# Kernel tuning notes

Hardware: AMD Instinct MI355X
Metric: run time of the kernel (lower is better)

The kernel has to match this reference:

```python
import jax, jax.numpy as jnp
import numpy as np

B, NVARS, H, D_MODEL = 16, 32, 128, 128
N_HEADS, MERGE = 8, 2
HEAD_DIM = D_MODEL // N_HEADS
D_FF = 256
ALPHA = 0.3
EPS = 1e-5  # BatchNorm1d default eps


def make_ema(T, alpha):
    # row i: E[i,0]=(1-a)^i, E[i,j]=a*(1-a)^(i-j) for 1<=j<=i, 0 above diagonal
    i = np.arange(T)
    diff = i[:, None] - i[None, :]
    E = np.where(diff >= 0, alpha * (1.0 - alpha) ** np.maximum(diff, 0), 0.0)
    E[:, 0] = (1.0 - alpha) ** i
    return jnp.asarray(E, dtype=jnp.float32)


def batchnorm(x, gamma, beta):
    # x: [BN, L, C]; torch does Transpose(1,2)->BatchNorm1d(C)->Transpose(1,2),
    # i.e. normalize each channel over (batch, length) with biased variance (train mode).
    mean = x.mean(axis=(0, 1), keepdims=True)
    var = x.var(axis=(0, 1), keepdims=True)
    return (x - mean) * jax.lax.rsqrt(var + EPS) * gamma + beta


def merge_heads(x):
    # x: [B, N, heads, T, d]. Torch: reshape(B*N, heads*T, d) then
    # rearrange '(hl1 hl2 hl3) d -> hl2 (hl3 hl1) d' with hl1=heads//MERGE, hl2=T, hl3=MERGE,
    # then reshape(B*N, T, heads*d).
    b, n, h, t, d = x.shape
    hl1 = h // MERGE
    y = x.reshape(b * n, hl1, t, MERGE, d)
    y = y.transpose(0, 2, 3, 1, 4).reshape(b * n, t, h * d)
    return y


def setup_inputs() -> dict:
    key = jax.random.key(0)
    ks = jax.random.split(key, 8)
    s = lambda fan_in: 1.0 / np.sqrt(fan_in)
    return {
        "src": jax.random.normal(ks[0], (B, NVARS, H, D_MODEL), jnp.float32),
        "qkv_w": jax.random.normal(ks[1], (D_MODEL, 3 * D_MODEL), jnp.float32) * s(D_MODEL),
        "qkv_b": jnp.zeros((3 * D_MODEL,), jnp.float32),
        "ff1_w1": jax.random.normal(ks[2], (D_MODEL, D_FF), jnp.float32) * s(D_MODEL),
        "ff1_b1": jnp.zeros((D_FF,), jnp.float32),
        "ff1_w2": jax.random.normal(ks[3], (D_FF, D_MODEL), jnp.float32) * s(D_FF),
        "ff1_b2": jnp.zeros((D_MODEL,), jnp.float32),
        "ff2_w1": jax.random.normal(ks[4], (D_MODEL, D_FF), jnp.float32) * s(D_MODEL),
        "ff2_b1": jnp.zeros((D_FF,), jnp.float32),
        "ff2_w2": jax.random.normal(ks[5], (D_FF, D_MODEL), jnp.float32) * s(D_FF),
        "ff2_b2": jnp.zeros((D_MODEL,), jnp.float32),
        "g1": jnp.ones((D_MODEL,), jnp.float32), "b1": jnp.zeros((D_MODEL,), jnp.float32),
        "g2": jnp.ones((D_MODEL,), jnp.float32), "b2": jnp.zeros((D_MODEL,), jnp.float32),
        "g3": jnp.ones((D_MODEL,), jnp.float32), "b3": jnp.zeros((D_MODEL,), jnp.float32),
        "ema_mat": make_ema(H, ALPHA),
    }


def reference(src, qkv_w, qkv_b, ff1_w1, ff1_b1, ff1_w2, ff1_b2,
              ff2_w1, ff2_b1, ff2_w2, ff2_b2, g1, b1, g2, b2, g3, b3, ema_mat):
    Bc, Nc, T, C = src.shape
    qkv = (src @ qkv_w + qkv_b).reshape(Bc, Nc, T, 3, N_HEADS, HEAD_DIM)
    qkv = jnp.transpose(qkv, (3, 0, 1, 4, 2, 5))  # [3, B, N, heads, T, d]
    q, k, v = qkv[0], qkv[1], qkv[2]

    E = ema_mat[:T, :T]
    ema = lambda x: jnp.einsum('bnhad,ga->bnhgd', x, E)

    # NB: original divides by head_dim**(-0.5), i.e. multiplies by sqrt(head_dim)
    s_tok = jnp.einsum('bnhed,bnhfd->bnhef', ema(q), ema(k)) * (HEAD_DIM ** 0.5)
    a_tok = jax.nn.softmax(s_tok, axis=-1)            # dropout p=0 (eval)
    o_tok = jnp.einsum('bnhef,bnhfd->bnhed', a_tok, v)  # [B,N,h,T,d]

    # hidden-dim attention: scores are [d,d], contracted over tokens; scale by sqrt(T)
    s_hid = jnp.einsum('bnhae,bnhaf->bnhef', q, k) * (T ** 0.5)
    a_hid = jax.nn.softmax(s_hid, axis=-1)
    o_hid = jnp.einsum('bnhef,bnhaf->bnhae', a_hid, v)  # [B,N,h,T,d]

    out1 = batchnorm(merge_heads(o_tok), g1, b1).reshape(Bc, Nc, T, C)
    out2 = batchnorm(merge_heads(o_hid), g2, b2).reshape(Bc, Nc, T, C)

    ff = lambda x, w1, bb1, w2, bb2: jax.nn.gelu(x @ w1 + bb1, approximate=False) @ w2 + bb2
    src2 = ff(out1, ff1_w1, ff1_b1, ff1_w2, ff1_b2) + ff(out2, ff2_w1, ff2_b1, ff2_w2, ff2_b2)

    out = src + src2
    out = batchnorm(out.reshape(Bc * Nc, T, C), g3, b3).reshape(Bc, Nc, T, C)
    return out
```

## Files before the change

kernel.cpp:

```cpp
#include <hip/hip_runtime.h>
#include <math.h>

#define BN_ 512
#define T_  128
#define C_  128
#define H_  8
#define D_  16
#define F_  256
#define M_  65536

typedef __bf16 bf16x8 __attribute__((ext_vector_type(8)));
typedef float f32x4 __attribute__((ext_vector_type(4)));
union U8 { uint2 d[2]; bf16x8 v; unsigned short u[8]; };

__device__ inline unsigned short f2bf(float x) {
  union { float f; unsigned int u; } a; a.f = x;
  unsigned int r = a.u + 0x7fffu + ((a.u >> 16) & 1u);
  return (unsigned short)(r >> 16);
}
__device__ inline float bf2f(unsigned short h) {
  return __uint_as_float((unsigned int)h << 16);
}
__device__ inline float gelu_f(float x) {
  float z  = x * 0.70710678118654752f;
  float az = fabsf(z);
  float t  = 1.0f / (1.0f + 0.3275911f * az);
  float poly = ((((1.061405429f*t - 1.453152027f)*t + 1.421413741f)*t
                 - 0.284496736f)*t + 0.254829592f)*t;
  float e  = __expf(-z*z);
  float er = 1.0f - poly*e;
  er = (z < 0.0f) ? -er : er;
  return 0.5f * x * (1.0f + er);
}

__global__ __launch_bounds__(256, 4) void k_qkv(
    const float* __restrict__ src, const unsigned short* __restrict__ wqh,
    const unsigned short* __restrict__ wql, const float* __restrict__ bias,
    float* __restrict__ qb, float* __restrict__ kb, float* __restrict__ vb) {
  __shared__ __align__(16) unsigned short Ah[8*512], Al[8*512];
  const int tid = threadIdx.x;
  const int lane = tid & 63, w = tid >> 6;
  const int cl = lane & 15, g = lane >> 4;
  const size_t rb = (size_t)blockIdx.x * 32;

  #pragma unroll
  for (int it=0; it<4; ++it) {
    int idx = it*256 + tid;
    int r = idx >> 5, c4 = (idx & 31)*4;
    float4 v = *(const float4*)&src[(rb + r)*128 + c4];
    float vv[4] = {v.x, v.y, v.z, v.w};
    int s = c4 >> 5, kl = c4 & 31;
    int g2 = (kl >> 2) & 3, j0 = (kl >> 4) << 2;
    int fi = ((r>>4)*4 + s)*512 + (g2*16 + (r & 15))*8 + j0;
    unsigned short h4[4], l4[4];
    #pragma unroll
    for (int e=0;e<4;++e) {
      h4[e] = f2bf(vv[e]);
      l4[e] = f2bf(vv[e] - bf2f(h4[e]));
    }
    *(uint2*)&Ah[fi] = make_uint2((unsigned)h4[0] | ((unsigned)h4[1]<<16),
                                  (unsigned)h4[2] | ((unsigned)h4[3]<<16));
    *(uint2*)&Al[fi] = make_uint2((unsigned)l4[0] | ((unsigned)l4[1]<<16),
                                  (unsigned)l4[2] | ((unsigned)l4[3]<<16));
  }
  __syncthreads();

  f32x4 acc[2][6];
  #pragma unroll
  for (int m=0;m<2;++m)
    #pragma unroll
    for (int n=0;n<6;++n) acc[m][n] = 0;

  #pragma unroll
  for (int s=0; s<4; ++s) {
    bf16x8 ah[2], al[2];
    #pragma unroll
    for (int m=0;m<2;++m) {
      ah[m] = *(const bf16x8*)&Ah[(m*4+s)*512 + lane*8];
      al[m] = *(const bf16x8*)&Al[(m*4+s)*512 + lane*8];
    }
    #pragma unroll
    for (int nt=0; nt<6; ++nt) {
      int n = w*96 + nt*16 + cl;
      size_t fi = (size_t)((s*384 + n)*4 + g)*8;
      bf16x8 bh = *(const bf16x8*)(wqh + fi);
      bf16x8 bl = *(const bf16x8*)(wql + fi);
      #pragma unroll
      for (int m=0;m<2;++m) {
        acc[m][nt] = __builtin_amdgcn_mfma_f32_16x16x32_bf16(ah[m], bh, acc[m][nt], 0,0,0);
        acc[m][nt] = __builtin_amdgcn_mfma_f32_16x16x32_bf16(ah[m], bl, acc[m][nt], 0,0,0);
        acc[m][nt] = __builtin_amdgcn_mfma_f32_16x16x32_bf16(al[m], bh, acc[m][nt], 0,0,0);
      }
    }
  }

  #pragma unroll
  for (int nt=0; nt<6; ++nt) {
    int n = w*96 + nt*16 + cl;
    int which = n >> 7, loc = n & 127;
    int h = loc >> 4, d = loc & 15;
    float* outb = (which==0) ? qb : ((which==1) ? kb : vb);
    float bv = bias[n];
    #pragma unroll
    for (int m=0;m<2;++m) {
      #pragma unroll
      for (int r=0;r<4;++r) {
        size_t row = rb + m*16 + g*4 + r;
        int bn = (int)(row >> 7), t = (int)(row & 127);
        outb[(((size_t)(bn*8 + h))*128 + t)*16 + d] = acc[m][nt][r] + bv;
      }
    }
  }
}

__global__ __launch_bounds__(256, 4) void k_attn(
    const float* __restrict__ qb, const float* __restrict__ kb,
    const float* __restrict__ vb, const unsigned short* __restrict__ ef,
    unsigned short* __restrict__ o1b, unsigned short* __restrict__ o2b,
    float* __restrict__ p12) {
  __shared__ __align__(16) unsigned short QFh[2048], QFl[2048];
  __shared__ __align__(16) unsigned short KFh[2048], KFl[2048];
  __shared__ __align__(16) unsigned short VF[2048];
  __shared__ __align__(16) unsigned short Vn[128*20];
  __shared__ __align__(16) unsigned short eqL[128*20], ekL[128*20];
  __shared__ __align__(16) float s2L[16*17];
  __shared__ float part[128];
  const int tid = threadIdx.x;
  const int lane = tid & 63, w = tid >> 6;
  const int cl = lane & 15, g = lane >> 4;
  const int bn = blockIdx.x >> 3, h = blockIdx.x & 7;
  const int h1 = h >> 1, hb = h & 1;
  const size_t base = (size_t)(bn*8 + h) * 2048;

  if (tid < 128) part[tid] = 0.f;

  {
    const int t = tid >> 1, d0 = (tid & 1) * 8;
    const int s = t >> 5, kk = t & 31;
    const int g2 = (kk >> 2) & 3;
    const int j = ((kk >> 4) << 2) | (kk & 3);
    const float* qp = &qb[base + t*16 + d0];
    const float* kp = &kb[base + t*16 + d0];
    const float* vp = &vb[base + t*16 + d0];
    float4 qa = *(const float4*)qp, qc = *(const float4*)(qp+4);
    float4 ka = *(const float4*)kp, kc = *(const float4*)(kp+4);
    float4 va = *(const float4*)vp, vc = *(const float4*)(vp+4);
    float qv[8] = {qa.x,qa.y,qa.z,qa.w,qc.x,qc.y,qc.z,qc.w};
    float kv[8] = {ka.x,ka.y,ka.z,ka.w,kc.x,kc.y,kc.z,kc.w};
    float vv[8] = {va.x,va.y,va.z,va.w,vc.x,vc.y,vc.z,vc.w};
    unsigned short vh[8];
    #pragma unroll
    for (int e2=0;e2<8;++e2) {
      int fi = s*512 + (g2*16 + d0 + e2)*8 + j;
      unsigned short qh = f2bf(qv[e2]);
      QFh[fi] = qh; QFl[fi] = f2bf(qv[e2] - bf2f(qh));
      unsigned short kh = f2bf(kv[e2]);
      KFh[fi] = kh; KFl[fi] = f2bf(kv[e2] - bf2f(kh));
      vh[e2] = f2bf(vv[e2]);
      VF[fi] = vh[e2];
    }
    unsigned int p0 = (unsigned)vh[0] | ((unsigned)vh[1]<<16);
    unsigned int p1 = (unsigned)vh[2] | ((unsigned)vh[3]<<16);
    unsigned int p2 = (unsigned)vh[4] | ((unsigned)vh[5]<<16);
    unsigned int p3 = (unsigned)vh[6] | ((unsigned)vh[7]<<16);
    *(uint2*)&Vn[t*20 + d0]     = make_uint2(p0,p1);
    *(uint2*)&Vn[t*20 + d0 + 4] = make_uint2(p2,p3);
  }
  __syncthreads();

  {
    f32x4 aq[2], ak[2];
    #pragma unroll
    for (int m=0;m<2;++m){ aq[m]=0; ak[m]=0; }
    #pragma unroll
    for (int s=0;s<4;++s) {
      bf16x8 qf = *(const bf16x8*)&QFh[s*512 + lane*8];
      bf16x8 kf = *(const bf16x8*)&KFh[s*512 + lane*8];
      #pragma unroll
      for (int m=0;m<2;++m) {
        int mt = w*2 + m;
        bf16x8 eA = *(const bf16x8*)&ef[(size_t)((mt*4 + s)*64 + lane)*8];
        aq[m] = __builtin_amdgcn_mfma_f32_16x16x32_bf16(eA, qf, aq[m], 0,0,0);
        ak[m] = __builtin_amdgcn_mfma_f32_16x16x32_bf16(eA, kf, ak[m], 0,0,0);
      }
    }
    #pragma unroll
    for (int m=0;m<2;++m)
      #pragma unroll
      for (int r=0;r<4;++r) {
        int row = w*32 + m*16 + g*4 + r;
        eqL[row*20 + cl] = f2bf(aq[m][r]);
        ekL[row*20 + cl] = f2bf(ak[m][r]);
      }
  }
  if (w == 3) {
    f32x4 a2; a2 = 0;
    #pragma unroll
    for (int s=0;s<4;++s) {
      bf16x8 qh = *(const bf16x8*)&QFh[s*512 + lane*8];
      bf16x8 ql = *(const bf16x8*)&QFl[s*512 + lane*8];
      bf16x8 kh = *(const bf16x8*)&KFh[s*512 + lane*8];
      bf16x8 kl = *(const bf16x8*)&KFl[s*512 + lane*8];
      a2 = __builtin_amdgcn_mfma_f32_16x16x32_bf16(qh, kh, a2, 0,0,0);
      a2 = __builtin_amdgcn_mfma_f32_16x16x32_bf16(qh, kl, a2, 0,0,0);
      a2 = __builtin_amdgcn_mfma_f32_16x16x32_bf16(ql, kh, a2, 0,0,0);
    }
    #pragma unroll
    for (int r=0;r<4;++r) {
      float sv = a2[r] * 11.313708498984761f;
      float mx = sv;
      mx = fmaxf(mx, __shfl_xor(mx, 1));
      mx = fmaxf(mx, __shfl_xor(mx, 2));
      mx = fmaxf(mx, __shfl_xor(mx, 4));
      mx = fmaxf(mx, __shfl_xor(mx, 8));
      float p = __expf(sv - mx);
      float sum = p;
      sum += __shfl_xor(sum, 1);
      sum += __shfl_xor(sum, 2);
      sum += __shfl_xor(sum, 4);
      sum += __shfl_xor(sum, 8);
      s2L[(g*4 + r)*17 + cl] = p / sum;
    }
  }
  __syncthreads();

  {
    f32x4 accS[8][2];
    #pragma unroll
    for (int kt=0;kt<8;++kt)
      #pragma unroll
      for (int qt=0;qt<2;++qt) accS[kt][qt] = 0;
    U8 eb[2];
    #pragma unroll
    for (int qt=0;qt<2;++qt) {
      eb[qt].d[0] = *(const uint2*)&eqL[(w*32 + qt*16 + cl)*20 + 4*g];
      eb[qt].d[1] = make_uint2(0,0);
    }
    #pragma unroll
    for (int kt=0;kt<8;++kt) {
      U8 ea;
      ea.d[0] = *(const uint2*)&ekL[(kt*16 + cl)*20 + 4*g];
      ea.d[1] = make_uint2(0,0);
      #pragma unroll
      for (int qt=0;qt<2;++qt)
        accS[kt][qt] = __builtin_amdgcn_mfma_f32_16x16x32_bf16(ea.v, eb[qt].v, accS[kt][qt], 0,0,0);
    }
    bf16x8 vfr[4];
    #pragma unroll
    for (int s=0;s<4;++s) vfr[s] = *(const bf16x8*)&VF[s*512 + lane*8];
    #pragma unroll
    for (int qt=0;qt<2;++qt) {
      float mx = -1e30f;
      #pragma unroll
      for (int kt=0;kt<8;++kt)
        #pragma unroll
        for (int r=0;r<4;++r) {
          accS[kt][qt][r] *= 4.0f;
          mx = fmaxf(mx, accS[kt][qt][r]);
        }
      mx = fmaxf(mx, __shfl_xor(mx, 16));
      mx = fmaxf(mx, __shfl_xor(mx, 32));
      float sum = 0.f;
      #pragma unroll
      for (int kt=0;kt<8;++kt)
        #pragma unroll
        for (int r=0;r<4;++r) {
          float p = __expf(accS[kt][qt][r] - mx);
          accS[kt][qt][r] = p; sum += p;
        }
      sum += __shfl_xor(sum, 16);
      sum += __shfl_xor(sum, 32);
      float inv = 1.0f / sum;
      f32x4 o; o = 0;
      #pragma unroll
      for (int s=0;s<4;++s) {
        U8 pa;
        #pragma unroll
        for (int j=0;j<8;++j)
          pa.u[j] = f2bf(accS[2*s + (j>>2)][qt][j&3] * inv);
        o = __builtin_amdgcn_mfma_f32_16x16x32_bf16(pa.v, vfr[s], o, 0,0,0);
      }
      #pragma unroll
      for (int r=0;r<4;++r) {
        int e = w*32 + qt*16 + g*4 + r;
        int t2 = hb*64 + (e>>1), cb = (e&1)*64 + h1*16 + cl;
        o1b[((size_t)(bn*128 + t2))*128 + cb] = f2bf(o[r]);
      }
      float s0 = o[0]+o[2], q0 = o[0]*o[0]+o[2]*o[2];
      float s1 = o[1]+o[3], q1 = o[1]*o[1]+o[3]*o[3];
      s0 += __shfl_xor(s0,16); s0 += __shfl_xor(s0,32);
      q0 += __shfl_xor(q0,16); q0 += __shfl_xor(q0,32);
      s1 += __shfl_xor(s1,16); s1 += __shfl_xor(s1,32);
      q1 += __shfl_xor(q1,16); q1 += __shfl_xor(q1,32);
      if (g == 0) {
        atomicAdd(&part[cl],      s0);
        atomicAdd(&part[16+cl],   q0);
        atomicAdd(&part[32+cl],   s1);
        atomicAdd(&part[48+cl],   q1);
      }
    }
  }

  {
    U8 bb;
    #pragma unroll
    for (int j=0;j<4;++j) bb.u[j] = f2bf(s2L[cl*17 + 4*g + j]);
    bb.d[1] = make_uint2(0,0);
    #pragma unroll
    for (int m=0;m<2;++m) {
      int tt = w*2 + m;
      U8 va;
      va.d[0] = *(const uint2*)&Vn[(tt*16 + cl)*20 + 4*g];
      va.d[1] = make_uint2(0,0);
      f32x4 o; o = 0;
      o = __builtin_amdgcn_mfma_f32_16x16x32_bf16(va.v, bb.v, o, 0,0,0);
      #pragma unroll
      for (int r=0;r<4;++r) {
        int t = tt*16 + g*4 + r;
        int t2 = hb*64 + (t>>1), cb = (t&1)*64 + h1*16 + cl;
        o2b[((size_t)(bn*128 + t2))*128 + cb] = f2bf(o[r]);
      }
      float s0 = o[0]+o[2], q0 = o[0]*o[0]+o[2]*o[2];
      float s1 = o[1]+o[3], q1 = o[1]*o[1]+o[3]*o[3];
      s0 += __shfl_xor(s0,16); s0 += __shfl_xor(s0,32);
      q0 += __shfl_xor(q0,16); q0 += __shfl_xor(q0,32);
      s1 += __shfl_xor(s1,16); s1 += __shfl_xor(s1,32);
      q1 += __shfl_xor(q1,16); q1 += __shfl_xor(q1,32);
      if (g == 0) {
        atomicAdd(&part[64+cl],    s0);
        atomicAdd(&part[64+16+cl], q0);
        atomicAdd(&part[64+32+cl], s1);
        atomicAdd(&part[64+48+cl], q1);
      }
    }
  }
  __syncthreads();
  if (tid < 128) p12[(size_t)blockIdx.x*128 + tid] = part[tid];
}

__global__ __launch_bounds__(256) void k_red12(
    const float* __restrict__ p12, float* __restrict__ q12) {
  __shared__ float red[256];
  const int tid = threadIdx.x;
  const int slot = tid & 127, half = tid >> 7;
  const int h = blockIdx.x & 7, chunk = blockIdx.x >> 3;
  float s = 0.f;
  for (int t = half; t < 32; t += 2)
    s += p12[(size_t)((chunk*32 + t)*8 + h)*128 + slot];
  red[tid] = s;
  __syncthreads();
  if (tid < 128)
    q12[(size_t)blockIdx.x*128 + tid] = red[tid] + red[tid + 128];
}

__global__ __launch_bounds__(256) void k_fin12(
    const float* __restrict__ q12,
    const float* __restrict__ g1, const float* __restrict__ b1,
    const float* __restrict__ g2, const float* __restrict__ b2,
    float* __restrict__ stats) {
  const int tid = threadIdx.x;
  const int br = tid >> 7, c = tid & 127;
  const int grp = c >> 6, h1 = (c & 63) >> 4, cl = c & 15;
  const int slot = br*64 + grp*32 + cl;
  float s = 0.f, q = 0.f;
  #pragma unroll 4
  for (int chunk = 0; chunk < 16; ++chunk) {
    const float* p0 = &q12[(size_t)(chunk*8 + h1*2)*128];
    s += p0[slot]      + p0[128 + slot];
    q += p0[slot + 16] + p0[128 + slot + 16];
  }
  const float inv = 1.0f/65536.0f;
  float m = s*inv, v = q*inv - m*m;
  float r = rsqrtf(v + 1e-5f);
  float gv = br ? g2[c] : g1[c];
  float bv = br ? b2[c] : b1[c];
  float sc = r * gv;
  stats[br*256 + c]       = sc;
  stats[br*256 + 128 + c] = bv - m*sc;
}

__global__ __launch_bounds__(256) void k_prep(
    const float* __restrict__ w11, const float* __restrict__ w12,
    const float* __restrict__ w21, const float* __restrict__ w22,
    const float* __restrict__ ema, const float* __restrict__ qkvw,
    unsigned short* __restrict__ wf, unsigned short* __restrict__ ef,
    unsigned short* __restrict__ wqh, unsigned short* __restrict__ wql) {
  if (blockIdx.x >= 72) {
    int tid3 = (blockIdx.x - 72)*256 + threadIdx.x;
    int s = tid3 / 1536;
    int rem = tid3 - s*1536;
    int n = rem >> 2, g = rem & 3;
    size_t fi = (size_t)((s*384 + n)*4 + g)*8;
    #pragma unroll
    for (int j=0;j<8;++j) {
      int k = 32*s + 16*(j>>2) + 4*g + (j&3);
      float v = qkvw[(size_t)k*384 + n];
      unsigned short h = f2bf(v);
      wqh[fi+j] = h;
      wql[fi+j] = f2bf(v - bf2f(h));
    }
    return;
  }
  if (blockIdx.x >= 64) {
    int tid2 = (blockIdx.x - 64)*256 + threadIdx.x;
    int mt = tid2 >> 8, s = (tid2 >> 6) & 3, lane = tid2 & 63;
    int cl = lane & 15, g = lane >> 4;
    unsigned short* dst = ef + (size_t)tid2*8;
    #pragma unroll
    for (int j=0;j<8;++j) {
      int k = 32*s + 16*(j>>2) + 4*g + (j&3);
      dst[j] = f2bf(ema[(size_t)(mt*16 + cl)*128 + k]);
    }
    return;
  }
  int tid = blockIdx.x*256 + threadIdx.x;
  int m = tid >> 12;
  int idx = tid & 4095;
  const float* w; int N;
  if (m==0)      { w = w11; N = 256; }
  else if (m==1) { w = w12; N = 128; }
  else if (m==2) { w = w21; N = 256; }
  else           { w = w22; N = 128; }
  int g  = idx & 3;
  int sn = idx >> 2;
  int n  = (N==256) ? (sn & 255) : (sn & 127);
  int s  = (N==256) ? (sn >> 8)  : (sn >> 7);
  unsigned short* dst = wf + m*32768 + idx*8;
  #pragma unroll
  for (int j=0; j<8; ++j) {
    int k = s*32 + g*4 + (j&3) + 16*(j>>2);
    dst[j] = f2bf(w[(size_t)k*N + n]);
  }
}

__global__ void k_ff(
    const unsigned short* __restrict__ o1b, const unsigned short* __restrict__ o2b,
    const float* __restrict__ src,
    const float* __restrict__ bb11, const float* __restrict__ bb12,
    const float* __restrict__ bb21, const float* __restrict__ bb22,
    const unsigned short* __restrict__ wf,
    const float* __restrict__ stats, float* __restrict__ outp,
    float* __restrict__ p3) {
  __shared__ __align__(16) unsigned short Xbf[64*128];
  __shared__ __align__(16) unsigned short Hbf[64*128];
  const int tid = threadIdx.x;
  const int lane = tid & 63, w = tid >> 6;
  const int cl = lane & 15, g = lane >> 4;
  const size_t rb = (size_t)blockIdx.x * 64;

  f32x4 acc2[4];
  #pragma unroll
  for (int m=0;m<4;++m) acc2[m] = 0;

  for (int br=0; br<2; ++br) {
    const unsigned short* xin = br ? o2b : o1b;
    const float* sc_ = stats + br*256;
    const float* sh_ = sc_ + 128;
    const unsigned short* w1f = wf + br*65536;
    const unsigned short* w2f = w1f + 32768;
    const float* b1g = br ? bb21 : bb11;

    __syncthreads();
    #pragma unroll
    for (int it=0; it<4; ++it) {
      int idx = it*512 + tid;
      int row = idx >> 5, c4 = (idx & 31)*4;
      uint2 u = *(const uint2*)&xin[(rb+row)*128 + c4];
      float x0 = bf2f((unsigned short)(u.x & 0xffff));
      float x1 = bf2f((unsigned short)(u.x >> 16));
      float x2 = bf2f((unsigned short)(u.y & 0xffff));
      float x3 = bf2f((unsigned short)(u.y >> 16));
      unsigned int lo = f2bf(fmaf(x0, sc_[c4+0], sh_[c4+0]))
                      | ((unsigned int)f2bf(fmaf(x1, sc_[c4+1], sh_[c4+1])) << 16);
      unsigned int hi = f2bf(fmaf(x2, sc_[c4+2], sh_[c4+2]))
                      | ((unsigned int)f2bf(fmaf(x3, sc_[c4+3], sh_[c4+3])) << 16);
      unsigned int byteo = (unsigned)((row*256 + c4*2) ^ ((row&7)<<4));
      *(uint2*)((char*)Xbf + byteo) = make_uint2(lo, hi);
    }
    __syncthreads();

    #pragma unroll
    for (int hc=0; hc<2; ++hc) {
      f32x4 acc1[4];
      #pragma unroll
      for (int m=0;m<4;++m) acc1[m] = 0;

      bf16x8 bfs[4];
      #pragma unroll
      for (int s=0; s<4; ++s) {
        int n = hc*128 + w*16 + cl;
        bfs[s] = *(const bf16x8*)(w1f + (size_t)((s*256 + n)*4 + g)*8);
      }
      #pragma unroll
      for (int s=0; s<4; ++s) {
        #pragma unroll
        for (int m=0; m<4; ++m) {
          int row = m*16 + cl;
          U8 u;
          u.d[0] = *(uint2*)((char*)Xbf + (unsigned)((row*256 + (s*32 + g*4)*2)    ^ ((row&7)<<4)));
          u.d[1] = *(uint2*)((char*)Xbf + (unsigned)((row*256 + (s*32 +16+ g*4)*2) ^ ((row&7)<<4)));
          acc1[m] = __builtin_amdgcn_mfma_f32_16x16x32_bf16(u.v, bfs[s], acc1[m], 0, 0, 0);
        }
      }

      {
        int col = w*16 + cl;
        float bias = b1g[hc*128 + col];
        #pragma unroll
        for (int m=0; m<4; ++m) {
          #pragma unroll
          for (int r=0; r<4; ++r) {
            float y = gelu_f(acc1[m][r] + bias);
            int row = m*16 + g*4 + r;
            unsigned int byteo = (unsigned)((row*256 + col*2) ^ ((row&7)<<4));
            *(unsigned short*)((char*)Hbf + byteo) = f2bf(y);
          }
        }
      }
      __syncthreads();

      bf16x8 bf2[4];
      #pragma unroll
      for (int s2l=0; s2l<4; ++s2l) {
        int s2 = hc*4 + s2l;
        int n = w*16 + cl;
        bf2[s2l] = *(const bf16x8*)(w2f + (size_t)((s2*128 + n)*4 + g)*8);
      }
      #pragma unroll
      for (int s2l=0; s2l<4; ++s2l) {
        #pragma unroll
        for (int m=0; m<4; ++m) {
          int row = m*16 + cl;
          U8 u;
          u.d[0] = *(uint2*)((char*)Hbf + (unsigned)((row*256 + (s2l*32 + g*4)*2)    ^ ((row&7)<<4)));
          u.d[1] = *(uint2*)((char*)Hbf + (unsigned)((row*256 + (s2l*32 +16+ g*4)*2) ^ ((row&7)<<4)));
          acc2[m] = __builtin_amdgcn_mfma_f32_16x16x32_bf16(u.v, bf2[s2l], acc2[m], 0, 0, 0);
        }
      }
      __syncthreads();
    }
  }

  {
    int col = w*16 + cl;
    float bias = bb12[col] + bb22[col];
    float cs = 0.f, cq = 0.f;
    #pragma unroll
    for (int m=0; m<4; ++m) {
      #pragma unroll
      for (int r=0; r<4; ++r) {
        size_t row = rb + m*16 + g*4 + r;
        float o = src[row*128 + col] + acc2[m][r] + bias;
        outp[row*128 + col] = o;
        cs += o; cq = fmaf(o, o, cq);
      }
    }
    cs += __shfl_down(cs, 32); cs += __shfl_down(cs, 16);
    cq += __shfl_down(cq, 32); cq += __shfl_down(cq, 16);
    if (g == 0) {
      p3[(size_t)blockIdx.x*256 + col]       = cs;
      p3[(size_t)blockIdx.x*256 + 128 + col] = cq;
    }
  }
}

__global__ __launch_bounds__(256) void k_red3(
    const float* __restrict__ p3, float* __restrict__ q3) {
  const int tid = threadIdx.x;
  float s = 0.f;
  const int b0 = blockIdx.x*32;
  for (int b = b0; b < b0 + 32; ++b)
    s += p3[(size_t)b*256 + tid];
  q3[(size_t)blockIdx.x*256 + tid] = s;
}

__global__ __launch_bounds__(256) void k_fin3(
    const float* __restrict__ q3, const float* __restrict__ g3,
    const float* __restrict__ b3, float* __restrict__ stats) {
  __shared__ float acc[256];
  const int tid = threadIdx.x;
  float s = 0.f;
  #pragma unroll 4
  for (int i = 0; i < 32; ++i) s += q3[i*256 + tid];
  acc[tid] = s;
  __syncthreads();
  if (tid < 128) {
    const float inv = 1.0f/65536.0f;
    float m = acc[tid]*inv, v = acc[128+tid]*inv - m*m;
    float r = rsqrtf(v + 1e-5f);
    float scv = r*g3[tid];
    stats[512 + tid] = scv;
    stats[640 + tid] = b3[tid] - m*scv;
  }
}

__global__ __launch_bounds__(256) void k_bn3(
    float* __restrict__ outp, const float* __restrict__ stats) {
  const int i0 = blockIdx.x*256 + threadIdx.x;
  #pragma unroll
  for (int it=0; it<4; ++it) {
    size_t fi = ((size_t)i0 + (size_t)it*524288) * 4;
    int c = (int)(fi & 127);
    float4 v = *(float4*)&outp[fi];
    v.x = fmaf(v.x, stats[512+c+0], stats[640+c+0]);
    v.y = fmaf(v.y, stats[512+c+1], stats[640+c+1]);
    v.z = fmaf(v.z, stats[512+c+2], stats[640+c+2]);
    v.w = fmaf(v.w, stats[512+c+3], stats[640+c+3]);
    *(float4*)&outp[fi] = v;
  }
}

extern "C" void kernel_launch(void* const* d_in, const int* in_sizes, int n_in,
                              void* d_out, int out_size, void* d_ws, size_t ws_size,
                              hipStream_t stream) {
  const float* src   = (const float*)d_in[0];
  const float* qkv_w = (const float*)d_in[1];
  const float* qkv_b = (const float*)d_in[2];
  const float* ff1w1 = (const float*)d_in[3];
  const float* ff1b1 = (const float*)d_in[4];
  const float* ff1w2 = (const float*)d_in[5];
  const float* ff1b2 = (const float*)d_in[6];
  const float* ff2w1 = (const float*)d_in[7];
  const float* ff2b1 = (const float*)d_in[8];
  const float* ff2w2 = (const float*)d_in[9];
  const float* ff2b2 = (const float*)d_in[10];
  const float* g1 = (const float*)d_in[11];
  const float* b1 = (const float*)d_in[12];
  const float* g2 = (const float*)d_in[13];
  const float* b2 = (const float*)d_in[14];
  const float* g3 = (const float*)d_in[15];
  const float* b3 = (const float*)d_in[16];
  const float* ema = (const float*)d_in[17];

  float* ws = (float*)d_ws;
  float* qb  = ws;
  float* kb  = qb + 8388608;
  float* vb  = kb + 8388608;
  unsigned short* o1b = (unsigned short*)(vb + 8388608);
  unsigned short* o2b = o1b + 8388608;
  float* p12 = (float*)(o2b + 8388608);
  float* p3  = p12 + 524288;
  float* stats = p3 + 262144;
  unsigned short* wfrag = (unsigned short*)(stats + 1024);
  unsigned short* efrag = wfrag + 131072;
  unsigned short* wqh   = efrag + 16384;
  unsigned short* wql   = wqh + 49152;
  float* q12 = (float*)(wql + 49152);
  float* q3  = q12 + 16384;
  float* outp = (float*)d_out;

  k_prep<<<dim3(96), dim3(256), 0, stream>>>(ff1w1, ff1w2, ff2w1, ff2w2, ema,
                                             qkv_w, wfrag, efrag, wqh, wql);
  k_qkv<<<dim3(2048), dim3(256), 0, stream>>>(src, wqh, wql, qkv_b, qb, kb, vb);
  k_attn<<<dim3(4096), dim3(256), 0, stream>>>(qb, kb, vb, efrag, o1b, o2b, p12);
  k_red12<<<dim3(128), dim3(256), 0, stream>>>(p12, q12);
  k_fin12<<<dim3(1), dim3(256), 0, stream>>>(q12, g1, b1, g2, b2, stats);
  k_ff<<<dim3(1024), dim3(512), 0, stream>>>(o1b, o2b, src,
      ff1b1, ff1b2, ff2b1, ff2b2, wfrag, stats, outp, p3);
  k_red3<<<dim3(32), dim3(256), 0, stream>>>(p3, q3);
  k_fin3<<<dim3(1), dim3(256), 0, stream>>>(q3, g3, b3, stats);
  k_bn3<<<dim3(2048), dim3(256), 0, stream>>>(outp, stats);
}
```

Before: 210.0 us.

## Fuse QKV projection into attention kernel, dropping fp32 q/k/v round trip

The QKV projection kernel is merged into the attention kernel. Each block now computes the Q, K and V columns for its own (bn, head) directly from src and writes them as bf16 fragments into shared memory, so the fp32 q/k/v buffers are never stored to or read back from global memory. Block indices are remapped so that the 8 heads of one bn run on nearby blocks, which should let src rows be reused from cache. In exchange, src is read once per head (eight times in total), each block does more work, and shared memory use grows through the pooled staging buffers, which may lower occupancy.

```diff
diff --git a/kernel.cpp b/kernel.cpp
--- a/kernel.cpp
+++ b/kernel.cpp
@@ -33,138 +33,97 @@
   return 0.5f * x * (1.0f + er);
 }
 
-__global__ __launch_bounds__(256, 4) void k_qkv(
-    const float* __restrict__ src, const unsigned short* __restrict__ wqh,
-    const unsigned short* __restrict__ wql, const float* __restrict__ bias,
-    float* __restrict__ qb, float* __restrict__ kb, float* __restrict__ vb) {
-  __shared__ __align__(16) unsigned short Ah[8*512], Al[8*512];
-  const int tid = threadIdx.x;
-  const int lane = tid & 63, w = tid >> 6;
-  const int cl = lane & 15, g = lane >> 4;
-  const size_t rb = (size_t)blockIdx.x * 32;
-
-  #pragma unroll
-  for (int it=0; it<4; ++it) {
-    int idx = it*256 + tid;
-    int r = idx >> 5, c4 = (idx & 31)*4;
-    float4 v = *(const float4*)&src[(rb + r)*128 + c4];
-    float vv[4] = {v.x, v.y, v.z, v.w};
-    int s = c4 >> 5, kl = c4 & 31;
-    int g2 = (kl >> 2) & 3, j0 = (kl >> 4) << 2;
-    int fi = ((r>>4)*4 + s)*512 + (g2*16 + (r & 15))*8 + j0;
-    unsigned short h4[4], l4[4];
-    #pragma unroll
-    for (int e=0;e<4;++e) {
-      h4[e] = f2bf(vv[e]);
-      l4[e] = f2bf(vv[e] - bf2f(h4[e]));
-    }
-    *(uint2*)&Ah[fi] = make_uint2((unsigned)h4[0] | ((unsigned)h4[1]<<16),
-                                  (unsigned)h4[2] | ((unsigned)h4[3]<<16));
-    *(uint2*)&Al[fi] = make_uint2((unsigned)l4[0] | ((unsigned)l4[1]<<16),
-                                  (unsigned)l4[2] | ((unsigned)l4[3]<<16));
-  }
-  __syncthreads();
-
-  f32x4 acc[2][6];
-  #pragma unroll
-  for (int m=0;m<2;++m)
-    #pragma unroll
-    for (int n=0;n<6;++n) acc[m][n] = 0;
-
-  #pragma unroll
-  for (int s=0; s<4; ++s) {
-    bf16x8 ah[2], al[2];
-    #pragma unroll
-    for (int m=0;m<2;++m) {
-      ah[m] = *(const bf16x8*)&Ah[(m*4+s)*512 + lane*8];
-      al[m] = *(const bf16x8*)&Al[(m*4+s)*512 + lane*8];
-    }
-    #pragma unroll
-    for (int nt=0; nt<6; ++nt) {
-      int n = w*96 + nt*16 + cl;
-      size_t fi = (size_t)((s*384 + n)*4 + g)*8;
-      bf16x8 bh = *(const bf16x8*)(wqh + fi);
-      bf16x8 bl = *(const bf16x8*)(wql + fi);
-      #pragma unroll
-      for (int m=0;m<2;++m) {
-        acc[m][nt] = __builtin_amdgcn_mfma_f32_16x16x32_bf16(ah[m], bh, acc[m][nt], 0,0,0);
-        acc[m][nt] = __builtin_amdgcn_mfma_f32_16x16x32_bf16(ah[m], bl, acc[m][nt], 0,0,0);
-        acc[m][nt] = __builtin_amdgcn_mfma_f32_16x16x32_bf16(al[m], bh, acc[m][nt], 0,0,0);
-      }
-    }
-  }
-
-  #pragma unroll
-  for (int nt=0; nt<6; ++nt) {
-    int n = w*96 + nt*16 + cl;
-    int which = n >> 7, loc = n & 127;
-    int h = loc >> 4, d = loc & 15;
-    float* outb = (which==0) ? qb : ((which==1) ? kb : vb);
-    float bv = bias[n];
-    #pragma unroll
-    for (int m=0;m<2;++m) {
-      #pragma unroll
-      for (int r=0;r<4;++r) {
-        size_t row = rb + m*16 + g*4 + r;
-        int bn = (int)(row >> 7), t = (int)(row & 127);
-        outb[(((size_t)(bn*8 + h))*128 + t)*16 + d] = acc[m][nt][r] + bv;
-      }
-    }
-  }
-}
-
-__global__ __launch_bounds__(256, 4) void k_attn(
-    const float* __restrict__ qb, const float* __restrict__ kb,
-    const float* __restrict__ vb, const unsigned short* __restrict__ ef,
+__global__ void k_qa(
+    const float* __restrict__ src,
+    const unsigned short* __restrict__ wqh, const unsigned short* __restrict__ wql,
+    const float* __restrict__ qbias, const unsigned short* __restrict__ ef,
     unsigned short* __restrict__ o1b, unsigned short* __restrict__ o2b,
     float* __restrict__ p12) {
+  __shared__ __align__(16) char pool[32768];
   __shared__ __align__(16) unsigned short QFh[2048], QFl[2048];
   __shared__ __align__(16) unsigned short KFh[2048], KFl[2048];
   __shared__ __align__(16) unsigned short VF[2048];
   __shared__ __align__(16) unsigned short Vn[128*20];
-  __shared__ __align__(16) unsigned short eqL[128*20], ekL[128*20];
   __shared__ __align__(16) float s2L[16*17];
   __shared__ float part[128];
+  unsigned short* Ah = (unsigned short*)pool;
+  unsigned short* Al = (unsigned short*)(pool + 16384);
+  unsigned short* eqL = (unsigned short*)pool;
+  unsigned short* ekL = (unsigned short*)(pool + 5120);
+
   const int tid = threadIdx.x;
   const int lane = tid & 63, w = tid >> 6;
   const int cl = lane & 15, g = lane >> 4;
-  const int bn = blockIdx.x >> 3, h = blockIdx.x & 7;
+  const int bid = blockIdx.x;
+  const int bn = (bid & 7)*64 + (bid >> 6);
+  const int h  = (bid >> 3) & 7;
   const int h1 = h >> 1, hb = h & 1;
-  const size_t base = (size_t)(bn*8 + h) * 2048;
 
   if (tid < 128) part[tid] = 0.f;
 
-  {
-    const int t = tid >> 1, d0 = (tid & 1) * 8;
-    const int s = t >> 5, kk = t & 31;
-    const int g2 = (kk >> 2) & 3;
-    const int j = ((kk >> 4) << 2) | (kk & 3);
-    const float* qp = &qb[base + t*16 + d0];
-    const float* kp = &kb[base + t*16 + d0];
-    const float* vp = &vb[base + t*16 + d0];
-    float4 qa = *(const float4*)qp, qc = *(const float4*)(qp+4);
-    float4 ka = *(const float4*)kp, kc = *(const float4*)(kp+4);
-    float4 va = *(const float4*)vp, vc = *(const float4*)(vp+4);
-    float qv[8] = {qa.x,qa.y,qa.z,qa.w,qc.x,qc.y,qc.z,qc.w};
-    float kv[8] = {ka.x,ka.y,ka.z,ka.w,kc.x,kc.y,kc.z,kc.w};
-    float vv[8] = {va.x,va.y,va.z,va.w,vc.x,vc.y,vc.z,vc.w};
-    unsigned short vh[8];
-    #pragma unroll
-    for (int e2=0;e2<8;++e2) {
-      int fi = s*512 + (g2*16 + d0 + e2)*8 + j;
-      unsigned short qh = f2bf(qv[e2]);
-      QFh[fi] = qh; QFl[fi] = f2bf(qv[e2] - bf2f(qh));
-      unsigned short kh = f2bf(kv[e2]);
-      KFh[fi] = kh; KFl[fi] = f2bf(kv[e2] - bf2f(kh));
-      vh[e2] = f2bf(vv[e2]);
-      VF[fi] = vh[e2];
-    }
-    unsigned int p0 = (unsigned)vh[0] | ((unsigned)vh[1]<<16);
-    unsigned int p1 = (unsigned)vh[2] | ((unsigned)vh[3]<<16);
-    unsigned int p2 = (unsigned)vh[4] | ((unsigned)vh[5]<<16);
-    unsigned int p3 = (unsigned)vh[6] | ((unsigned)vh[7]<<16);
-    *(uint2*)&Vn[t*20 + d0]     = make_uint2(p0,p1);
-    *(uint2*)&Vn[t*20 + d0 + 4] = make_uint2(p2,p3);
+  const float bq = qbias[h*16 + cl];
+  const float bk = qbias[128 + h*16 + cl];
+  const float bv = qbias[256 + h*16 + cl];
+  for (int half = 0; half < 2; ++half) {
+    __syncthreads();
+    #pragma unroll
+    for (int it=0; it<8; ++it) {
+      int idx = it*256 + tid;
+      int r = idx >> 5, c4 = (idx & 31)*4;
+      float4 v = *(const float4*)&src[(size_t)(bn*128 + half*64 + r)*128 + c4];
+      float vv[4] = {v.x, v.y, v.z, v.w};
+      int s = c4 >> 5, kl = c4 & 31;
+      int g2 = (kl >> 2) & 3, j0 = (kl >> 4) << 2;
+      int fi = ((r>>4)*4 + s)*512 + (g2*16 + (r & 15))*8 + j0;
+      unsigned short h4[4], l4[4];
+      #pragma unroll
+      for (int e=0;e<4;++e) {
+        h4[e] = f2bf(vv[e]);
+        l4[e] = f2bf(vv[e] - bf2f(h4[e]));
+      }
+      *(uint2*)&Ah[fi] = make_uint2((unsigned)h4[0] | ((unsigned)h4[1]<<16),
+                                    (unsigned)h4[2] | ((unsigned)h4[3]<<16));
+      *(uint2*)&Al[fi] = make_uint2((unsigned)l4[0] | ((unsigned)l4[1]<<16),
+                                    (unsigned)l4[2] | ((unsigned)l4[3]<<16));
+    }
+    __syncthreads();
+
+    f32x4 acc[3];
+    #pragma unroll
+    for (int nt=0; nt<3; ++nt) acc[nt] = 0;
+    #pragma unroll
+    for (int s=0; s<4; ++s) {
+      bf16x8 ah = *(const bf16x8*)&Ah[(w*4+s)*512 + lane*8];
+      bf16x8 al = *(const bf16x8*)&Al[(w*4+s)*512 + lane*8];
+      #pragma unroll
+      for (int nt=0; nt<3; ++nt) {
+        int n = nt*128 + h*16 + cl;
+        size_t fi = (size_t)((s*384 + n)*4 + g)*8;
+        bf16x8 bh = *(const bf16x8*)(wqh + fi);
+        bf16x8 bl = *(const bf16x8*)(wql + fi);
+        acc[nt] = __builtin_amdgcn_mfma_f32_16x16x32_bf16(ah, bh, acc[nt], 0,0,0);
+        acc[nt] = __builtin_amdgcn_mfma_f32_16x16x32_bf16(ah, bl, acc[nt], 0,0,0);
+        acc[nt] = __builtin_amdgcn_mfma_f32_16x16x32_bf16(al, bh, acc[nt], 0,0,0);
+      }
+    }
+    const int tb = half*64 + w*16 + g*4;
+    #pragma unroll
+    for (int r=0; r<4; ++r) {
+      int t = tb + r;
+      int s_t = t >> 5, kk = t & 31;
+      int g2 = (kk >> 2) & 3, j = ((kk >> 4) << 2) | (kk & 3);
+      int fi = s_t*512 + (g2*16 + cl)*8 + j;
+      float qv = acc[0][r] + bq;
+      unsigned short qh = f2bf(qv);
+      QFh[fi] = qh; QFl[fi] = f2bf(qv - bf2f(qh));
+      float kv = acc[1][r] + bk;
+      unsigned short kh = f2bf(kv);
+      KFh[fi] = kh; KFl[fi] = f2bf(kv - bf2f(kh));
+      float vv = acc[2][r] + bv;
+      unsigned short vh = f2bf(vv);
+      VF[fi] = vh;
+      Vn[t*20 + cl] = vh;
+    }
   }
   __syncthreads();
 
@@ -335,7 +294,7 @@
     }
   }
   __syncthreads();
-  if (tid < 128) p12[(size_t)blockIdx.x*128 + tid] = part[tid];
+  if (tid < 128) p12[(size_t)(bn*8 + h)*128 + tid] = part[tid];
 }
 
 __global__ __launch_bounds__(256) void k_red12(
@@ -633,10 +592,7 @@
   const float* ema = (const float*)d_in[17];
 
   float* ws = (float*)d_ws;
-  float* qb  = ws;
-  float* kb  = qb + 8388608;
-  float* vb  = kb + 8388608;
-  unsigned short* o1b = (unsigned short*)(vb + 8388608);
+  unsigned short* o1b = (unsigned short*)ws;
   unsigned short* o2b = o1b + 8388608;
   float* p12 = (float*)(o2b + 8388608);
   float* p3  = p12 + 524288;
@@ -651,8 +607,8 @@
 
   k_prep<<<dim3(96), dim3(256), 0, stream>>>(ff1w1, ff1w2, ff2w1, ff2w2, ema,
                                              qkv_w, wfrag, efrag, wqh, wql);
-  k_qkv<<<dim3(2048), dim3(256), 0, stream>>>(src, wqh, wql, qkv_b, qb, kb, vb);
-  k_attn<<<dim3(4096), dim3(256), 0, stream>>>(qb, kb, vb, efrag, o1b, o2b, p12);
+  k_qa<<<dim3(4096), dim3(256), 0, stream>>>(src, wqh, wql, qkv_b, efrag,
+                                             o1b, o2b, p12);
   k_red12<<<dim3(128), dim3(256), 0, stream>>>(p12, q12);
   k_fin12<<<dim3(1), dim3(256), 0, stream>>>(q12, g1, b1, g2, b2, stats);
   k_ff<<<dim3(1024), dim3(512), 0, stream>>>(o1b, o2b, src,
```

Result: slower. 261.9 us (+24.7%).
